# Performance work log

Hardware: AMD Instinct MI355X
Metric: run time of the kernel (lower is better)

## Reference

```python
import jax, jax.numpy as jnp
import numpy as np

B, N, D = 64, 4096, 256


def setup_inputs() -> dict:
    key = jax.random.key(0)
    k1, k2, k3 = jax.random.split(key, 3)
    x = jax.random.normal(k1, (B, D), dtype=jnp.float32)
    z = jax.random.normal(k2, (B, D), dtype=jnp.float32)
    means = jax.random.normal(k3, (B, N, D), dtype=jnp.float32)
    precision = jnp.eye(D, dtype=jnp.float32)  # matches torch init: nn.Parameter(torch.eye(mem_dim))
    return {"x": x, "z": z, "means": means, "precision": precision, "iterations": 10}


def reference(x, z, means, precision, iterations):
    # EM-like iterative soft-assignment: Mahalanobis distances -> softmax weights -> weighted mean.
    def step(z, _):
        diff = means - z[:, None, :]                                  # [B, N, D]
        quad = jnp.einsum('bnd,de,bne->bn', diff, precision, diff)    # [B, N] quadratic forms
        w = jax.nn.softmax(-0.5 * quad, axis=1)                       # [B, N]
        z_new = jnp.einsum('bn,bnd->bd', w, means)                    # [B, D]
        return z_new, None

    z_final, _ = jax.lax.scan(step, z, None, length=iterations)
    return z_final
```

## Files before the change

kernel.cpp:

```cpp
#include <hip/hip_runtime.h>
#include <hip/hip_fp16.h>
#include <hip/hip_cooperative_groups.h>
#include <math.h>

namespace cg = cooperative_groups;

constexpr int B_ = 64;
constexpr int N_ = 4096;
constexpr int D_ = 256;
constexpr int NCH = 64;
constexpr int NPB = N_ / NCH;
constexpr int NPW = NPB / 4;
constexpr int NSTEP = NPW / 4;

typedef float f4v __attribute__((ext_vector_type(4)));
__device__ __forceinline__ float4 nt_load4(const float4* p) {
    f4v v = __builtin_nontemporal_load((const f4v*)p);
    return make_float4(v.x, v.y, v.z, v.w);
}

__global__ __launch_bounds__(256) void flag_kernel(const float* __restrict__ P,
                                                   int* __restrict__ flag) {
    __shared__ int sh[256];
    const int tid = threadIdx.x;
    int bad = 0;
    for (int i = tid; i < D_ * D_; i += 256) {
        const int r = i >> 8, c = i & 255;
        const float expect = (r == c) ? 1.0f : 0.0f;
        bad |= (P[i] != expect) ? 1 : 0;
    }
    sh[tid] = bad;
    __syncthreads();
    for (int s = 128; s > 0; s >>= 1) {
        if (tid < s) sh[tid] |= sh[tid + s];
        __syncthreads();
    }
    if (tid == 0) *flag = sh[0];
}

#define SCORE_AND_UPDATE()                                                     \
    {                                                                          \
        float p_ = 0.f;                                                        \
        _Pragma("unroll")                                                      \
        for (int j = 0; j < 4; j++) {                                          \
            p_ += m[j].x * (vr[j].x - m[j].x);                                 \
            p_ += m[j].y * (vr[j].y - m[j].y);                                 \
            p_ += m[j].z * (vr[j].z - m[j].z);                                 \
            p_ += m[j].w * (vr[j].w - m[j].w);                                 \
        }                                                                      \
        p_ += __shfl_xor(p_, 1, 64);                                           \
        p_ += __shfl_xor(p_, 2, 64);                                           \
        p_ += __shfl_xor(p_, 4, 64);                                           \
        p_ += __shfl_xor(p_, 8, 64);                                           \
        float s_ = 0.5f * p_;                                                  \
        if (flg) {                \
            __syncthreads();                                                   \
            _Pragma("unroll")                                                  \
            for (int jj = 0; jj < 2; jj++)                                     \
                _Pragma("unroll")                                              \
                for (int h = 0; h < 2; h++)                                    \
                    ((float4*)&srows[wave][g][0])[q * 2 + 32 * jj + h] =       \
                        m[jj * 2 + h];                                         \
            __syncthreads();                                                   \
            float dl = 0.f;                                                    \
            for (int k = 0; k < 16; k++) {                                     \
                const int d_ = q * 16 + k;                                     \
                const float md = srows[wave][g][d_];                           \
                float pm = 0.f;                                                \
                for (int e = 0; e < D_; e++)                                   \
                    pm += P[d_ * D_ + e] * srows[wave][g][e];                  \
                dl += md * (md - pm);                                          \
            }                                                                  \
            dl += __shfl_xor(dl, 1, 64);                                       \
            dl += __shfl_xor(dl, 2, 64);                                       \
            dl += __shfl_xor(dl, 4, 64);                                       \
            dl += __shfl_xor(dl, 8, 64);                                       \
            s_ += 0.5f * dl;                                                   \
        }                                                                      \
        const float newM_ = fmaxf(runM, s_);                                   \
        const float sc_ = __expf(runM - newM_);                                \
        const float e_  = __expf(s_ - newM_);                                  \
        runS = fmaf(runS, sc_, e_);                                            \
        _Pragma("unroll")                                                      \
        for (int j = 0; j < 4; j++) {                                          \
            tacc[j].x = fmaf(tacc[j].x, sc_, e_ * m[j].x);                     \
            tacc[j].y = fmaf(tacc[j].y, sc_, e_ * m[j].y);                     \
            tacc[j].z = fmaf(tacc[j].z, sc_, e_ * m[j].z);                     \
            tacc[j].w = fmaf(tacc[j].w, sc_, e_ * m[j].w);                     \
        }                                                                      \
        runM = newM_;                                                          \
    }

#define FAST_SCORE_UPDATE()                                                    \
    {                                                                          \
        float p_ = 0.f;                                                        \
        _Pragma("unroll")                                                      \
        for (int j = 0; j < 4; j++) {                                          \
            p_ += m[j].x * (vr[j].x - m[j].x);                                 \
            p_ += m[j].y * (vr[j].y - m[j].y);                                 \
            p_ += m[j].z * (vr[j].z - m[j].z);                                 \
            p_ += m[j].w * (vr[j].w - m[j].w);                                 \
        }                                                                      \
        p_ += __shfl_xor(p_, 1, 64);                                           \
        p_ += __shfl_xor(p_, 2, 64);                                           \
        p_ += __shfl_xor(p_, 4, 64);                                           \
        p_ += __shfl_xor(p_, 8, 64);                                           \
        const float s_ = 0.5f * p_;                                            \
        const float newM_ = fmaxf(runM, s_);                                   \
        const float sc_ = __expf(runM - newM_);                                \
        const float e_  = __expf(s_ - newM_);                                  \
        runS = fmaf(runS, sc_, e_);                                            \
        _Pragma("unroll")                                                      \
        for (int j = 0; j < 4; j++) {                                          \
            tacc[j].x = fmaf(tacc[j].x, sc_, e_ * m[j].x);                     \
            tacc[j].y = fmaf(tacc[j].y, sc_, e_ * m[j].y);                     \
            tacc[j].z = fmaf(tacc[j].z, sc_, e_ * m[j].z);                     \
            tacc[j].w = fmaf(tacc[j].w, sc_, e_ * m[j].w);                     \
        }                                                                      \
        runM = newM_;                                                          \
    }

template <bool USE_H, int PARTS_>
__global__ __launch_bounds__(256) void persistent_kernel(
        const float* __restrict__ means, const float* __restrict__ z0,
        const float* __restrict__ P, const int* __restrict__ flag,
        __half* __restrict__ mh, float* __restrict__ pT,
        float2* __restrict__ pS, float* __restrict__ out) {
    constexpr int GRID = 64 * PARTS_;
    constexpr int RPB = N_ / PARTS_;
    constexpr int RPW = RPB / 4;
    constexpr int NSTEPS = RPW / 4;
    cg::grid_group grid = cg::this_grid();

    const int gid = blockIdx.x, bb = gid / PARTS_, part = gid % PARTS_;
    const int tid = threadIdx.x, wave = tid >> 6, lane = tid & 63;
    const int q = lane & 15, g = lane >> 4;

    __shared__ __align__(16) float vsh[D_];
    __shared__ __align__(16) float shbuf[4][D_];
    __shared__ __align__(16) float srows[4][4][D_];
    __shared__ __align__(16) float zsh[D_];
    __shared__ float wM[4], wS[4];

    const int flg = *flag;

    {
        const float zd = z0[bb * D_ + tid];
        if (!flg) {
            vsh[tid] = 2.f * zd;
        } else {
            zsh[tid] = zd;
            __syncthreads();
            float vv = 0.f;
            for (int e = 0; e < D_; e++)
                vv += (P[tid * D_ + e] + P[e * D_ + tid]) * zsh[e];
            vsh[tid] = vv;
        }
        __syncthreads();
    }

    const size_t wrowbase = (size_t)bb * N_ + (size_t)part * RPB + (size_t)wave * RPW;

    for (int t = 0; t < 10; t++) {
        float4 vr[4];
        #pragma unroll
        for (int jj = 0; jj < 2; jj++)
            #pragma unroll
            for (int h = 0; h < 2; h++)
                vr[jj * 2 + h] = ((const float4*)vsh)[q * 2 + 32 * jj + h];

        float runM = -INFINITY, runS = 0.f;
        float4 tacc[4];
        #pragma unroll
        for (int j = 0; j < 4; j++) tacc[j] = make_float4(0.f, 0.f, 0.f, 0.f);

        if (!flg) {
            if (USE_H && t > 0) {
                const __half* wb = mh + wrowbase * D_;
                float4 r0 = ((const float4*)(wb + (size_t)g * D_))[q];
                float4 r1 = ((const float4*)(wb + (size_t)g * D_))[q + 16];
                #pragma unroll 2
                for (int step = 0; step < NSTEPS; step++) {
                    const int pr = ((step + 1 < NSTEPS) ? step + 1 : step) * 4 + g;
                    const __half* rpn = wb + (size_t)pr * D_;
                    const float4 n0 = ((const float4*)rpn)[q];
                    const float4 n1 = ((const float4*)rpn)[q + 16];
                    float4 m[4];
                    {
                        const __half2* h0 = (const __half2*)&r0;
                        const float2 f0 = __half22float2(h0[0]);
                        const float2 f1 = __half22float2(h0[1]);
                        const float2 f2 = __half22float2(h0[2]);
                        const float2 f3 = __half22float2(h0[3]);
                        m[0] = make_float4(f0.x, f0.y, f1.x, f1.y);
                        m[1] = make_float4(f2.x, f2.y, f3.x, f3.y);
                        const __half2* h1 = (const __half2*)&r1;
                        const float2 g0 = __half22float2(h1[0]);
                        const float2 g1 = __half22float2(h1[1]);
                        const float2 g2 = __half22float2(h1[2]);
                        const float2 g3 = __half22float2(h1[3]);
                        m[2] = make_float4(g0.x, g0.y, g1.x, g1.y);
                        m[3] = make_float4(g2.x, g2.y, g3.x, g3.y);
                    }
                    FAST_SCORE_UPDATE()
                    r0 = n0; r1 = n1;
                }
            } else {
                const float* wb = means + wrowbase * D_;
                float4 m[4];
                {
                    const float4* rp = (const float4*)(wb + (size_t)g * D_);
                    m[0] = nt_load4(rp + q * 2);
                    m[1] = nt_load4(rp + q * 2 + 1);
                    m[2] = nt_load4(rp + q * 2 + 32);
                    m[3] = nt_load4(rp + q * 2 + 33);
                }
                #pragma unroll 2
                for (int step = 0; step < NSTEPS; step++) {
                    const int pr = ((step + 1 < NSTEPS) ? step + 1 : step) * 4 + g;
                    const float4* rpn = (const float4*)(wb + (size_t)pr * D_);
                    const float4 n0 = nt_load4(rpn + q * 2);
                    const float4 n1 = nt_load4(rpn + q * 2 + 1);
                    const float4 n2 = nt_load4(rpn + q * 2 + 32);
                    const float4 n3 = nt_load4(rpn + q * 2 + 33);
                    if (USE_H && t == 0) {
                        const int r = step * 4 + g;
                        __half* hp = mh + (wrowbase + r) * D_;
                        #pragma unroll
                        for (int jj = 0; jj < 2; jj++) {
                            union { uint4 u4; __half2 h2[4]; } pk;
                            pk.h2[0] = __floats2half2_rn(m[jj*2].x,   m[jj*2].y);
                            pk.h2[1] = __floats2half2_rn(m[jj*2].z,   m[jj*2].w);
                            pk.h2[2] = __floats2half2_rn(m[jj*2+1].x, m[jj*2+1].y);
                            pk.h2[3] = __floats2half2_rn(m[jj*2+1].z, m[jj*2+1].w);
                            *(uint4*)(hp + q * 8 + 128 * jj) = pk.u4;
                        }
                    }
                    FAST_SCORE_UPDATE()
                    m[0] = n0; m[1] = n1; m[2] = n2; m[3] = n3;
                }
            }
        } else {
            if (USE_H && t > 0) {
                for (int step = 0; step < NSTEPS; step++) {
                    const int r = step * 4 + g;
                    const __half* rp = mh + (wrowbase + r) * D_;
                    float4 m[4];
                    #pragma unroll
                    for (int jj = 0; jj < 2; jj++) {
                        float4 raw = ((const float4*)rp)[q + 16 * jj];
                        const __half2* hp2 = (const __half2*)&raw;
                        const float2 f0 = __half22float2(hp2[0]);
                        const float2 f1 = __half22float2(hp2[1]);
                        const float2 f2 = __half22float2(hp2[2]);
                        const float2 f3 = __half22float2(hp2[3]);
                        m[jj * 2 + 0] = make_float4(f0.x, f0.y, f1.x, f1.y);
                        m[jj * 2 + 1] = make_float4(f2.x, f2.y, f3.x, f3.y);
                    }
                    SCORE_AND_UPDATE()
                }
            } else {
                for (int step = 0; step < NSTEPS; step++) {
                    const int r = step * 4 + g;
                    const float* rp = means + (wrowbase + r) * D_;
                    float4 m[4];
                    #pragma unroll
                    for (int jj = 0; jj < 2; jj++)
                        #pragma unroll
                        for (int h = 0; h < 2; h++)
                            m[jj * 2 + h] = ((const float4*)rp)[q * 2 + 32 * jj + h];
                    if (USE_H && t == 0) {
                        __half* hp = mh + (wrowbase + r) * D_;
                        #pragma unroll
                        for (int jj = 0; jj < 2; jj++) {
                            union { uint4 u4; __half2 h2[4]; } pk;
                            pk.h2[0] = __floats2half2_rn(m[jj*2].x,   m[jj*2].y);
                            pk.h2[1] = __floats2half2_rn(m[jj*2].z,   m[jj*2].w);
                            pk.h2[2] = __floats2half2_rn(m[jj*2+1].x, m[jj*2+1].y);
                            pk.h2[3] = __floats2half2_rn(m[jj*2+1].z, m[jj*2+1].w);
                            *(uint4*)(hp + q * 8 + 128 * jj) = pk.u4;
                        }
                    }
                    SCORE_AND_UPDATE()
                }
            }
        }

        float Mw = runM;
        Mw = fmaxf(Mw, __shfl_xor(Mw, 16, 64));
        Mw = fmaxf(Mw, __shfl_xor(Mw, 32, 64));
        const float aw = __expf(runM - Mw);
        float Sa = runS * aw;
        Sa += __shfl_xor(Sa, 16, 64);
        Sa += __shfl_xor(Sa, 32, 64);
        #pragma unroll
        for (int j = 0; j < 4; j++) {
            tacc[j].x *= aw; tacc[j].y *= aw; tacc[j].z *= aw; tacc[j].w *= aw;
            tacc[j].x += __shfl_xor(tacc[j].x, 16, 64);
            tacc[j].y += __shfl_xor(tacc[j].y, 16, 64);
            tacc[j].z += __shfl_xor(tacc[j].z, 16, 64);
            tacc[j].w += __shfl_xor(tacc[j].w, 16, 64);
            tacc[j].x += __shfl_xor(tacc[j].x, 32, 64);
            tacc[j].y += __shfl_xor(tacc[j].y, 32, 64);
            tacc[j].z += __shfl_xor(tacc[j].z, 32, 64);
            tacc[j].w += __shfl_xor(tacc[j].w, 32, 64);
        }
        if (lane < 16) {
            #pragma unroll
            for (int j = 0; j < 4; j++)
                ((float4*)shbuf[wave])[q * 2 + 32 * (j >> 1) + (j & 1)] = tacc[j];
        }
        if (lane == 0) { wM[wave] = Mw; wS[wave] = Sa; }
        __syncthreads();
        const float Mb = fmaxf(fmaxf(wM[0], wM[1]), fmaxf(wM[2], wM[3]));
        const float a0 = __expf(wM[0] - Mb), a1 = __expf(wM[1] - Mb),
                    a2 = __expf(wM[2] - Mb), a3 = __expf(wM[3] - Mb);
        const float Tc = a0 * shbuf[0][tid] + a1 * shbuf[1][tid] +
                         a2 * shbuf[2][tid] + a3 * shbuf[3][tid];
        const int buf = t & 1;
        pT[((size_t)buf * GRID + gid) * D_ + tid] = Tc;
        if (tid == 0)
            pS[buf * GRID + gid] = make_float2(
                Mb, a0 * wS[0] + a1 * wS[1] + a2 * wS[2] + a3 * wS[3]);

        grid.sync();

        float Mg = -INFINITY;
        float2 stl[PARTS_];
        #pragma unroll
        for (int pI = 0; pI < PARTS_; pI++) {
            stl[pI] = pS[buf * GRID + bb * PARTS_ + pI];
            Mg = fmaxf(Mg, stl[pI].x);
        }
        float Sg = 0.f, accg = 0.f;
        #pragma unroll
        for (int pI = 0; pI < PARTS_; pI++) {
            const float a = __expf(stl[pI].x - Mg);
            Sg += a * stl[pI].y;
            accg += a * pT[((size_t)buf * GRID + bb * PARTS_ + pI) * D_ + tid];
        }
        const float zv = accg / Sg;
        if (t == 9) {
            if (part == 0) out[bb * D_ + tid] = zv;
        } else {
            if (!flg) {
                vsh[tid] = 2.f * zv;
            } else {
                zsh[tid] = zv;
                __syncthreads();
                float vv = 0.f;
                for (int e = 0; e < D_; e++)
                    vv += (P[tid * D_ + e] + P[e * D_ + tid]) * zsh[e];
                vsh[tid] = vv;
            }
            __syncthreads();
        }
    }
}

__global__ __launch_bounds__(256) void vcalc_kernel(const float* __restrict__ P,
                                                    const float* __restrict__ z,
                                                    const int* __restrict__ flag,
                                                    float* __restrict__ v) {
    __shared__ float zsh[D_];
    const int b = blockIdx.x, d = threadIdx.x;
    const float zd = z[b * D_ + d];
    if (*flag == 0) {
        v[b * D_ + d] = 2.0f * zd;
        return;
    }
    zsh[d] = zd;
    __syncthreads();
    float acc = 0.f;
    for (int e = 0; e < D_; e++)
        acc += (P[d * D_ + e] + P[e * D_ + d]) * zsh[e];
    v[b * D_ + d] = acc;
}

template <bool WRITE_H>
__global__ __launch_bounds__(256) void fused_f32_kernel(const float* __restrict__ means,
                                                        const float* __restrict__ v,
                                                        const float* __restrict__ P,
                                                        const int* __restrict__ flag,
                                                        __half* __restrict__ mh,
                                                        float* __restrict__ Tbuf,
                                                        float2* __restrict__ stats) {
    const int b = blockIdx.y, chunk = blockIdx.x;
    const int tid = threadIdx.x, wave = tid >> 6, lane = tid & 63;
    const int q = lane & 15, g = lane >> 4;
    __shared__ __align__(16) float vsh[D_];
    __shared__ __align__(16) float shbuf[4][D_];
    __shared__ __align__(16) float srows[4][4][D_];
    __shared__ float wM[4], wS[4];
    vsh[tid] = v[b * D_ + tid];
    __syncthreads();
    float4 vr[4];
    #pragma unroll
    for (int jj = 0; jj < 2; jj++)
        #pragma unroll
        for (int h = 0; h < 2; h++)
            vr[jj * 2 + h] = ((const float4*)vsh)[q * 2 + 32 * jj + h];
    const int flg = *flag;

    float runM = -INFINITY, runS = 0.f;
    float4 tacc[4];
    #pragma unroll
    for (int j = 0; j < 4; j++) tacc[j] = make_float4(0.f, 0.f, 0.f, 0.f);

    const size_t rowbase = (size_t)b * N_ + (size_t)chunk * NPB + (size_t)wave * NPW;

    for (int step = 0; step < NSTEP; step++) {
        const int r = step * 4 + g;
        const float* rp = means + (rowbase + r) * D_;
        float4 m[4];
        #pragma unroll
        for (int jj = 0; jj < 2; jj++)
            #pragma unroll
            for (int h = 0; h < 2; h++)
                m[jj * 2 + h] = ((const float4*)rp)[q * 2 + 32 * jj + h];
        if (WRITE_H) {
            __half* hp = mh + (rowbase + r) * D_;
            #pragma unroll
            for (int jj = 0; jj < 2; jj++) {
                union { uint4 u4; __half2 h2[4]; } pk;
                pk.h2[0] = __floats2half2_rn(m[jj*2].x,   m[jj*2].y);
                pk.h2[1] = __floats2half2_rn(m[jj*2].z,   m[jj*2].w);
                pk.h2[2] = __floats2half2_rn(m[jj*2+1].x, m[jj*2+1].y);
                pk.h2[3] = __floats2half2_rn(m[jj*2+1].z, m[jj*2+1].w);
                *(uint4*)(hp + q * 8 + 128 * jj) = pk.u4;
            }
        }
        SCORE_AND_UPDATE()
    }

    float Mw = runM;
    Mw = fmaxf(Mw, __shfl_xor(Mw, 16, 64));
    Mw = fmaxf(Mw, __shfl_xor(Mw, 32, 64));
    const float aw = __expf(runM - Mw);
    float Sa = runS * aw;
    Sa += __shfl_xor(Sa, 16, 64);
    Sa += __shfl_xor(Sa, 32, 64);
    #pragma unroll
    for (int j = 0; j < 4; j++) {
        tacc[j].x *= aw; tacc[j].y *= aw; tacc[j].z *= aw; tacc[j].w *= aw;
        tacc[j].x += __shfl_xor(tacc[j].x, 16, 64);
        tacc[j].y += __shfl_xor(tacc[j].y, 16, 64);
        tacc[j].z += __shfl_xor(tacc[j].z, 16, 64);
        tacc[j].w += __shfl_xor(tacc[j].w, 16, 64);
        tacc[j].x += __shfl_xor(tacc[j].x, 32, 64);
        tacc[j].y += __shfl_xor(tacc[j].y, 32, 64);
        tacc[j].z += __shfl_xor(tacc[j].z, 32, 64);
        tacc[j].w += __shfl_xor(tacc[j].w, 32, 64);
    }
    if (lane < 16) {
        #pragma unroll
        for (int j = 0; j < 4; j++)
            ((float4*)shbuf[wave])[q * 2 + 32 * (j >> 1) + (j & 1)] = tacc[j];
    }
    if (lane == 0) { wM[wave] = Mw; wS[wave] = Sa; }
    __syncthreads();
    const float Mb = fmaxf(fmaxf(wM[0], wM[1]), fmaxf(wM[2], wM[3]));
    const float a0 = __expf(wM[0] - Mb), a1 = __expf(wM[1] - Mb),
                a2 = __expf(wM[2] - Mb), a3 = __expf(wM[3] - Mb);
    const float Tc = a0 * shbuf[0][tid] + a1 * shbuf[1][tid] +
                     a2 * shbuf[2][tid] + a3 * shbuf[3][tid];
    Tbuf[((size_t)(b * NCH + chunk)) * D_ + tid] = Tc;
    if (tid == 0)
        stats[b * NCH + chunk] = make_float2(
            Mb, a0 * wS[0] + a1 * wS[1] + a2 * wS[2] + a3 * wS[3]);
}

__global__ __launch_bounds__(256) void fused_f16_kernel(const __half* __restrict__ mh,
                                                        const float* __restrict__ v,
                                                        const float* __restrict__ P,
                                                        const int* __restrict__ flag,
                                                        float* __restrict__ Tbuf,
                                                        float2* __restrict__ stats) {
    const int b = blockIdx.y, chunk = blockIdx.x;
    const int tid = threadIdx.x, wave = tid >> 6, lane = tid & 63;
    const int q = lane & 15, g = lane >> 4;
    __shared__ __align__(16) float vsh[D_];
    __shared__ __align__(16) float shbuf[4][D_];
    __shared__ __align__(16) float srows[4][4][D_];
    __shared__ float wM[4], wS[4];
    vsh[tid] = v[b * D_ + tid];
    __syncthreads();
    float4 vr[4];
    #pragma unroll
    for (int jj = 0; jj < 2; jj++)
        #pragma unroll
        for (int h = 0; h < 2; h++)
            vr[jj * 2 + h] = ((const float4*)vsh)[q * 2 + 32 * jj + h];
    const int flg = *flag;

    float runM = -INFINITY, runS = 0.f;
    float4 tacc[4];
    #pragma unroll
    for (int j = 0; j < 4; j++) tacc[j] = make_float4(0.f, 0.f, 0.f, 0.f);

    const size_t rowbase = (size_t)b * N_ + (size_t)chunk * NPB + (size_t)wave * NPW;

    for (int step = 0; step < NSTEP; step++) {
        const int r = step * 4 + g;
        const __half* rp = mh + (rowbase + r) * D_;
        float4 m[4];
        #pragma unroll
        for (int jj = 0; jj < 2; jj++) {
            float4 raw = ((const float4*)rp)[q + 16 * jj];
            const __half2* hp2 = (const __half2*)&raw;
            const float2 f0 = __half22float2(hp2[0]);
            const float2 f1 = __half22float2(hp2[1]);
            const float2 f2 = __half22float2(hp2[2]);
            const float2 f3 = __half22float2(hp2[3]);
            m[jj * 2 + 0] = make_float4(f0.x, f0.y, f1.x, f1.y);
            m[jj * 2 + 1] = make_float4(f2.x, f2.y, f3.x, f3.y);
        }
        SCORE_AND_UPDATE()
    }

    float Mw = runM;
    Mw = fmaxf(Mw, __shfl_xor(Mw, 16, 64));
    Mw = fmaxf(Mw, __shfl_xor(Mw, 32, 64));
    const float aw = __expf(runM - Mw);
    float Sa = runS * aw;
    Sa += __shfl_xor(Sa, 16, 64);
    Sa += __shfl_xor(Sa, 32, 64);
    #pragma unroll
    for (int j = 0; j < 4; j++) {
        tacc[j].x *= aw; tacc[j].y *= aw; tacc[j].z *= aw; tacc[j].w *= aw;
        tacc[j].x += __shfl_xor(tacc[j].x, 16, 64);
        tacc[j].y += __shfl_xor(tacc[j].y, 16, 64);
        tacc[j].z += __shfl_xor(tacc[j].z, 16, 64);
        tacc[j].w += __shfl_xor(tacc[j].w, 16, 64);
        tacc[j].x += __shfl_xor(tacc[j].x, 32, 64);
        tacc[j].y += __shfl_xor(tacc[j].y, 32, 64);
        tacc[j].z += __shfl_xor(tacc[j].z, 32, 64);
        tacc[j].w += __shfl_xor(tacc[j].w, 32, 64);
    }
    if (lane < 16) {
        #pragma unroll
        for (int j = 0; j < 4; j++)
            ((float4*)shbuf[wave])[q * 2 + 32 * (j >> 1) + (j & 1)] = tacc[j];
    }
    if (lane == 0) { wM[wave] = Mw; wS[wave] = Sa; }
    __syncthreads();
    const float Mb = fmaxf(fmaxf(wM[0], wM[1]), fmaxf(wM[2], wM[3]));
    const float a0 = __expf(wM[0] - Mb), a1 = __expf(wM[1] - Mb),
                a2 = __expf(wM[2] - Mb), a3 = __expf(wM[3] - Mb);
    const float Tc = a0 * shbuf[0][tid] + a1 * shbuf[1][tid] +
                     a2 * shbuf[2][tid] + a3 * shbuf[3][tid];
    Tbuf[((size_t)(b * NCH + chunk)) * D_ + tid] = Tc;
    if (tid == 0)
        stats[b * NCH + chunk] = make_float2(
            Mb, a0 * wS[0] + a1 * wS[1] + a2 * wS[2] + a3 * wS[3]);
}

__global__ __launch_bounds__(256) void combine_kernel(const float* __restrict__ Tbuf,
                                                      const float2* __restrict__ stats,
                                                      const float* __restrict__ P,
                                                      const int* __restrict__ flag,
                                                      float* __restrict__ v,
                                                      float* __restrict__ out) {
    const int b = blockIdx.x, d = threadIdx.x;
    __shared__ float Msh[NCH], Ssh[NCH];
    __shared__ float zsh[D_];
    if (d < NCH) {
        const float2 st = stats[b * NCH + d];
        Msh[d] = st.x; Ssh[d] = st.y;
    }
    __syncthreads();
    float M = -INFINITY;
    for (int c = 0; c < NCH; c++) M = fmaxf(M, Msh[c]);
    float S = 0.f, acc = 0.f;
    for (int c = 0; c < NCH; c++) {
        const float a = __expf(Msh[c] - M);
        S += a * Ssh[c];
        acc += a * Tbuf[((size_t)(b * NCH + c)) * D_ + d];
    }
    const float z = acc / S;
    if (out) out[b * D_ + d] = z;
    if (*flag == 0) {
        v[b * D_ + d] = 2.0f * z;
        return;
    }
    zsh[d] = z;
    __syncthreads();
    float vv = 0.f;
    for (int e = 0; e < D_; e++)
        vv += (P[d * D_ + e] + P[e * D_ + d]) * zsh[e];
    v[b * D_ + d] = vv;
}

extern "C" void kernel_launch(void* const* d_in, const int* in_sizes, int n_in,
                              void* d_out, int out_size, void* d_ws, size_t ws_size,
                              hipStream_t stream) {
    const float* z0    = (const float*)d_in[1];
    const float* means = (const float*)d_in[2];
    const float* P     = (const float*)d_in[3];
    float* out = (float*)d_out;

    char* ws = (char*)d_ws;
    size_t off = 0;
    int*    flag  = (int*)ws;                     off = 256;
    float*  v     = (float*)(ws + off);           off += (size_t)B_ * D_ * 4;
    float*  Tbuf  = (float*)(ws + off);           off += (size_t)B_ * NCH * D_ * 4;
    float2* stats = (float2*)(ws + off);          off += (size_t)B_ * NCH * 8;
    off = (off + 255) & ~(size_t)255;
    float*  pT    = (float*)(ws + off);           off += 2ull * 1024 * D_ * 4;
    float2* pS    = (float2*)(ws + off);          off += 2ull * 1024 * 8;
    off = (off + 255) & ~(size_t)255;
    __half* mh    = (__half*)(ws + off);
    const size_t coop_need  = off;
    const size_t full_need  = off + (size_t)B_ * N_ * D_ * 2;
    const bool use_h = (ws_size >= full_need);
    const bool ws_ok = (ws_size >= coop_need);

    flag_kernel<<<dim3(1), dim3(256), 0, stream>>>(P, flag);

    if (ws_ok) {
        void* args[] = {(void*)&means, (void*)&z0, (void*)&P, (void*)&flag,
                        (void*)&mh, (void*)&pT, (void*)&pS, (void*)&out};
        int nb = 0;
        if (use_h) {
            if (hipOccupancyMaxActiveBlocksPerMultiprocessor(
                    &nb, persistent_kernel<true, 16>, 256, 0) == hipSuccess && nb >= 4) {
                if (hipLaunchCooperativeKernel(persistent_kernel<true, 16>,
                        dim3(1024), dim3(256), args, 0, stream) == hipSuccess)
                    return;
            }
            nb = 0;
            if (hipOccupancyMaxActiveBlocksPerMultiprocessor(
                    &nb, persistent_kernel<true, 8>, 256, 0) == hipSuccess && nb >= 2) {
                if (hipLaunchCooperativeKernel(persistent_kernel<true, 8>,
                        dim3(512), dim3(256), args, 0, stream) == hipSuccess)
                    return;
            }
        } else {
            if (hipOccupancyMaxActiveBlocksPerMultiprocessor(
                    &nb, persistent_kernel<false, 16>, 256, 0) == hipSuccess && nb >= 4) {
                if (hipLaunchCooperativeKernel(persistent_kernel<false, 16>,
                        dim3(1024), dim3(256), args, 0, stream) == hipSuccess)
                    return;
            }
            nb = 0;
            if (hipOccupancyMaxActiveBlocksPerMultiprocessor(
                    &nb, persistent_kernel<false, 8>, 256, 0) == hipSuccess && nb >= 2) {
                if (hipLaunchCooperativeKernel(persistent_kernel<false, 8>,
                        dim3(512), dim3(256), args, 0, stream) == hipSuccess)
                    return;
            }
        }
    }

    vcalc_kernel<<<dim3(B_), dim3(256), 0, stream>>>(P, z0, flag, v);
    if (use_h) {
        fused_f32_kernel<true><<<dim3(NCH, B_), dim3(256), 0, stream>>>(
            means, v, P, flag, mh, Tbuf, stats);
        combine_kernel<<<dim3(B_), dim3(256), 0, stream>>>(Tbuf, stats, P, flag, v, nullptr);
        for (int t = 1; t < 10; t++) {
            fused_f16_kernel<<<dim3(NCH, B_), dim3(256), 0, stream>>>(
                mh, v, P, flag, Tbuf, stats);
            combine_kernel<<<dim3(B_), dim3(256), 0, stream>>>(Tbuf, stats, P, flag, v,
                                                               (t == 9) ? out : nullptr);
        }
    } else {
        for (int t = 0; t < 10; t++) {
            fused_f32_kernel<false><<<dim3(NCH, B_), dim3(256), 0, stream>>>(
                means, v, P, flag, nullptr, Tbuf, stats);
            combine_kernel<<<dim3(B_), dim3(256), 0, stream>>>(Tbuf, stats, P, flag, v,
                                                               (t == 9) ? out : nullptr);
        }
    }
}
```

Baseline: 731.6 us.

## Precompute mᵀPm per row, deepen fp16 prefetch, split FMA chains

Adds a separate kernel that precomputes 0.5·mᵀPm for every mean row when the precision matrix is not the identity. The slow path then needs only a dot product minus that constant, replacing its per-step O(D²) shared-memory matvec and barriers. The identity fast path gets a 4-deep register prefetch of fp16 rows and four independent FMA accumulators to shorten dependency chains. It also sets launch_bounds min-blocks to 4 and removes the srows shared buffer. Since the test uses an identity P, cn_kernel exits early and only the prefetch, FMA and occupancy changes affect timing, at the cost of one extra launch and more register pressure.

After: 1.460 ms. 99.6% more time.

```diff
diff --git a/kernel.cpp b/kernel.cpp
--- a/kernel.cpp
+++ b/kernel.cpp
@@ -12,11 +12,29 @@
 constexpr int NPB = N_ / NCH;
 constexpr int NPW = NPB / 4;
 constexpr int NSTEP = NPW / 4;
+constexpr int CNR = 16;
 
 typedef float f4v __attribute__((ext_vector_type(4)));
 __device__ __forceinline__ float4 nt_load4(const float4* p) {
     f4v v = __builtin_nontemporal_load((const f4v*)p);
     return make_float4(v.x, v.y, v.z, v.w);
+}
+
+__device__ __forceinline__ void cvt_h8(const float4 r0, const float4 r1, float4 m[4]) {
+    const __half2* h0 = (const __half2*)&r0;
+    const float2 f0 = __half22float2(h0[0]);
+    const float2 f1 = __half22float2(h0[1]);
+    const float2 f2 = __half22float2(h0[2]);
+    const float2 f3 = __half22float2(h0[3]);
+    m[0] = make_float4(f0.x, f0.y, f1.x, f1.y);
+    m[1] = make_float4(f2.x, f2.y, f3.x, f3.y);
+    const __half2* h1 = (const __half2*)&r1;
+    const float2 g0 = __half22float2(h1[0]);
+    const float2 g1 = __half22float2(h1[1]);
+    const float2 g2 = __half22float2(h1[2]);
+    const float2 g3 = __half22float2(h1[3]);
+    m[2] = make_float4(g0.x, g0.y, g1.x, g1.y);
+    m[3] = make_float4(g2.x, g2.y, g3.x, g3.y);
 }
 
 __global__ __launch_bounds__(256) void flag_kernel(const float* __restrict__ P,
@@ -37,6 +55,92 @@
     }
     if (tid == 0) *flag = sh[0];
 }
+
+__global__ __launch_bounds__(256) void cn_kernel(const float* __restrict__ means,
+                                                 const float* __restrict__ P,
+                                                 const int* __restrict__ flag,
+                                                 float* __restrict__ Cn) {
+    if (*flag == 0) return;
+    const int row0 = blockIdx.x * CNR;
+    const int d = threadIdx.x;
+    __shared__ __align__(16) float msh[CNR][D_];
+    __shared__ float red[CNR][4];
+    #pragma unroll
+    for (int i = 0; i < CNR; i++)
+        msh[i][d] = means[(size_t)(row0 + i) * D_ + d];
+    __syncthreads();
+    float acc[CNR];
+    #pragma unroll
+    for (int r = 0; r < CNR; r++) acc[r] = 0.f;
+    for (int e = 0; e < D_; e++) {
+        const float pde = P[d * D_ + e];
+        #pragma unroll
+        for (int r = 0; r < CNR; r++) acc[r] = fmaf(pde, msh[r][e], acc[r]);
+    }
+    const int lane = d & 63, wv = d >> 6;
+    #pragma unroll
+    for (int r = 0; r < CNR; r++) {
+        float pv = msh[r][d] * acc[r];
+        for (int s = 1; s < 64; s <<= 1) pv += __shfl_xor(pv, s, 64);
+        if (lane == 0) red[r][wv] = pv;
+    }
+    __syncthreads();
+    if (d < CNR)
+        Cn[row0 + d] = 0.5f * (red[d][0] + red[d][1] + red[d][2] + red[d][3]);
+}
+
+#define REDUCE16(P)                                                            \
+    P += __shfl_xor(P, 1, 64);                                                 \
+    P += __shfl_xor(P, 2, 64);                                                 \
+    P += __shfl_xor(P, 4, 64);                                                 \
+    P += __shfl_xor(P, 8, 64);
+
+#define ONLINE_UPDATE(SEXPR)                                                   \
+    {                                                                          \
+        const float s_ = (SEXPR);                                              \
+        const float newM_ = fmaxf(runM, s_);                                   \
+        const float sc_ = __expf(runM - newM_);                                \
+        const float e_  = __expf(s_ - newM_);                                  \
+        runS = fmaf(runS, sc_, e_);                                            \
+        _Pragma("unroll")                                                      \
+        for (int j = 0; j < 4; j++) {                                          \
+            tacc[j].x = fmaf(tacc[j].x, sc_, e_ * m[j].x);                     \
+            tacc[j].y = fmaf(tacc[j].y, sc_, e_ * m[j].y);                     \
+            tacc[j].z = fmaf(tacc[j].z, sc_, e_ * m[j].z);                     \
+            tacc[j].w = fmaf(tacc[j].w, sc_, e_ * m[j].w);                     \
+        }                                                                      \
+        runM = newM_;                                                          \
+    }
+
+#define FAST_SCORE_UPDATE()                                                    \
+    {                                                                          \
+        float pa = 0.f, pb = 0.f, pc2 = 0.f, pd = 0.f;                         \
+        _Pragma("unroll")                                                      \
+        for (int j = 0; j < 4; j++) {                                          \
+            pa  = fmaf(m[j].x, vr[j].x - m[j].x, pa);                          \
+            pb  = fmaf(m[j].y, vr[j].y - m[j].y, pb);                          \
+            pc2 = fmaf(m[j].z, vr[j].z - m[j].z, pc2);                         \
+            pd  = fmaf(m[j].w, vr[j].w - m[j].w, pd);                          \
+        }                                                                      \
+        float p_ = (pa + pb) + (pc2 + pd);                                     \
+        REDUCE16(p_)                                                           \
+        ONLINE_UPDATE(0.5f * p_)                                               \
+    }
+
+#define SLOW_SCORE_UPDATE(CV)                                                  \
+    {                                                                          \
+        float pa = 0.f, pb = 0.f, pc2 = 0.f, pd = 0.f;                         \
+        _Pragma("unroll")                                                      \
+        for (int j = 0; j < 4; j++) {                                          \
+            pa  = fmaf(m[j].x, vr[j].x, pa);                                   \
+            pb  = fmaf(m[j].y, vr[j].y, pb);                                   \
+            pc2 = fmaf(m[j].z, vr[j].z, pc2);                                  \
+            pd  = fmaf(m[j].w, vr[j].w, pd);                                   \
+        }                                                                      \
+        float p_ = (pa + pb) + (pc2 + pd);                                     \
+        REDUCE16(p_)                                                           \
+        ONLINE_UPDATE(0.5f * p_ - (CV))                                        \
+    }
 
 #define SCORE_AND_UPDATE()                                                     \
     {                                                                          \
@@ -53,7 +157,7 @@
         p_ += __shfl_xor(p_, 4, 64);                                           \
         p_ += __shfl_xor(p_, 8, 64);                                           \
         float s_ = 0.5f * p_;                                                  \
-        if (flg) {                \
+        if (flg) {                                                             \
             __syncthreads();                                                   \
             _Pragma("unroll")                                                  \
             for (int jj = 0; jj < 2; jj++)                                     \
@@ -91,41 +195,13 @@
         runM = newM_;                                                          \
     }
 
-#define FAST_SCORE_UPDATE()                                                    \
-    {                                                                          \
-        float p_ = 0.f;                                                        \
-        _Pragma("unroll")                                                      \
-        for (int j = 0; j < 4; j++) {                                          \
-            p_ += m[j].x * (vr[j].x - m[j].x);                                 \
-            p_ += m[j].y * (vr[j].y - m[j].y);                                 \
-            p_ += m[j].z * (vr[j].z - m[j].z);                                 \
-            p_ += m[j].w * (vr[j].w - m[j].w);                                 \
-        }                                                                      \
-        p_ += __shfl_xor(p_, 1, 64);                                           \
-        p_ += __shfl_xor(p_, 2, 64);                                           \
-        p_ += __shfl_xor(p_, 4, 64);                                           \
-        p_ += __shfl_xor(p_, 8, 64);                                           \
-        const float s_ = 0.5f * p_;                                            \
-        const float newM_ = fmaxf(runM, s_);                                   \
-        const float sc_ = __expf(runM - newM_);                                \
-        const float e_  = __expf(s_ - newM_);                                  \
-        runS = fmaf(runS, sc_, e_);                                            \
-        _Pragma("unroll")                                                      \
-        for (int j = 0; j < 4; j++) {                                          \
-            tacc[j].x = fmaf(tacc[j].x, sc_, e_ * m[j].x);                     \
-            tacc[j].y = fmaf(tacc[j].y, sc_, e_ * m[j].y);                     \
-            tacc[j].z = fmaf(tacc[j].z, sc_, e_ * m[j].z);                     \
-            tacc[j].w = fmaf(tacc[j].w, sc_, e_ * m[j].w);                     \
-        }                                                                      \
-        runM = newM_;                                                          \
-    }
-
 template <bool USE_H, int PARTS_>
-__global__ __launch_bounds__(256) void persistent_kernel(
+__global__ __launch_bounds__(256, 4) void persistent_kernel(
         const float* __restrict__ means, const float* __restrict__ z0,
         const float* __restrict__ P, const int* __restrict__ flag,
-        __half* __restrict__ mh, float* __restrict__ pT,
-        float2* __restrict__ pS, float* __restrict__ out) {
+        const float* __restrict__ Cn, __half* __restrict__ mh,
+        float* __restrict__ pT, float2* __restrict__ pS,
+        float* __restrict__ out) {
     constexpr int GRID = 64 * PARTS_;
     constexpr int RPB = N_ / PARTS_;
     constexpr int RPW = RPB / 4;
@@ -138,7 +214,6 @@
 
     __shared__ __align__(16) float vsh[D_];
     __shared__ __align__(16) float shbuf[4][D_];
-    __shared__ __align__(16) float srows[4][4][D_];
     __shared__ __align__(16) float zsh[D_];
     __shared__ float wM[4], wS[4];
 
@@ -177,52 +252,59 @@
         if (!flg) {
             if (USE_H && t > 0) {
                 const __half* wb = mh + wrowbase * D_;
-                float4 r0 = ((const float4*)(wb + (size_t)g * D_))[q];
-                float4 r1 = ((const float4*)(wb + (size_t)g * D_))[q + 16];
-                #pragma unroll 2
-                for (int step = 0; step < NSTEPS; step++) {
-                    const int pr = ((step + 1 < NSTEPS) ? step + 1 : step) * 4 + g;
-                    const __half* rpn = wb + (size_t)pr * D_;
-                    const float4 n0 = ((const float4*)rpn)[q];
-                    const float4 n1 = ((const float4*)rpn)[q + 16];
-                    float4 m[4];
-                    {
-                        const __half2* h0 = (const __half2*)&r0;
-                        const float2 f0 = __half22float2(h0[0]);
-                        const float2 f1 = __half22float2(h0[1]);
-                        const float2 f2 = __half22float2(h0[2]);
-                        const float2 f3 = __half22float2(h0[3]);
-                        m[0] = make_float4(f0.x, f0.y, f1.x, f1.y);
-                        m[1] = make_float4(f2.x, f2.y, f3.x, f3.y);
-                        const __half2* h1 = (const __half2*)&r1;
-                        const float2 g0 = __half22float2(h1[0]);
-                        const float2 g1 = __half22float2(h1[1]);
-                        const float2 g2 = __half22float2(h1[2]);
-                        const float2 g3 = __half22float2(h1[3]);
-                        m[2] = make_float4(g0.x, g0.y, g1.x, g1.y);
-                        m[3] = make_float4(g2.x, g2.y, g3.x, g3.y);
+                constexpr int PF = 4;
+                float4 pf0[PF], pf1[PF];
+                #pragma unroll
+                for (int i = 0; i < PF; i++) {
+                    const int rr = (i < NSTEPS ? i : NSTEPS - 1) * 4 + g;
+                    const __half* rp = wb + (size_t)rr * D_;
+                    pf0[i] = ((const float4*)rp)[q];
+                    pf1[i] = ((const float4*)rp)[q + 16];
+                }
+                for (int base = 0; base < NSTEPS; base += PF) {
+                    #pragma unroll
+                    for (int k = 0; k < PF; k++) {
+                        const int step = base + k;
+                        const float4 r0 = pf0[k], r1 = pf1[k];
+                        const int ps = (step + PF < NSTEPS) ? step + PF
+                                                            : NSTEPS - 1;
+                        const __half* rp = wb + (size_t)(ps * 4 + g) * D_;
+                        pf0[k] = ((const float4*)rp)[q];
+                        pf1[k] = ((const float4*)rp)[q + 16];
+                        float4 m[4];
+                        cvt_h8(r0, r1, m);
+                        FAST_SCORE_UPDATE()
                     }
-                    FAST_SCORE_UPDATE()
-                    r0 = n0; r1 = n1;
                 }
             } else {
                 const float* wb = means + wrowbase * D_;
                 float4 m[4];
                 {
                     const float4* rp = (const float4*)(wb + (size_t)g * D_);
-                    m[0] = nt_load4(rp + q * 2);
-                    m[1] = nt_load4(rp + q * 2 + 1);
-                    m[2] = nt_load4(rp + q * 2 + 32);
-                    m[3] = nt_load4(rp + q * 2 + 33);
+                    if (USE_H) {
+                        m[0] = nt_load4(rp + q * 2);
+                        m[1] = nt_load4(rp + q * 2 + 1);
+                        m[2] = nt_load4(rp + q * 2 + 32);
+                        m[3] = nt_load4(rp + q * 2 + 33);
+                    } else {
+                        m[0] = rp[q * 2];     m[1] = rp[q * 2 + 1];
+                        m[2] = rp[q * 2 + 32]; m[3] = rp[q * 2 + 33];
+                    }
                 }
                 #pragma unroll 2
                 for (int step = 0; step < NSTEPS; step++) {
                     const int pr = ((step + 1 < NSTEPS) ? step + 1 : step) * 4 + g;
                     const float4* rpn = (const float4*)(wb + (size_t)pr * D_);
-                    const float4 n0 = nt_load4(rpn + q * 2);
-                    const float4 n1 = nt_load4(rpn + q * 2 + 1);
-                    const float4 n2 = nt_load4(rpn + q * 2 + 32);
-                    const float4 n3 = nt_load4(rpn + q * 2 + 33);
+                    float4 n0, n1, n2, n3;
+                    if (USE_H) {
+                        n0 = nt_load4(rpn + q * 2);
+                        n1 = nt_load4(rpn + q * 2 + 1);
+                        n2 = nt_load4(rpn + q * 2 + 32);
+                        n3 = nt_load4(rpn + q * 2 + 33);
+                    } else {
+                        n0 = rpn[q * 2];     n1 = rpn[q * 2 + 1];
+                        n2 = rpn[q * 2 + 32]; n3 = rpn[q * 2 + 33];
+                    }
                     if (USE_H && t == 0) {
                         const int r = step * 4 + g;
                         __half* hp = mh + (wrowbase + r) * D_;
@@ -245,19 +327,12 @@
                 for (int step = 0; step < NSTEPS; step++) {
                     const int r = step * 4 + g;
                     const __half* rp = mh + (wrowbase + r) * D_;
+                    const float4 r0 = ((const float4*)rp)[q];
+                    const float4 r1 = ((const float4*)rp)[q + 16];
                     float4 m[4];
-                    #pragma unroll
-                    for (int jj = 0; jj < 2; jj++) {
-                        float4 raw = ((const float4*)rp)[q + 16 * jj];
-                        const __half2* hp2 = (const __half2*)&raw;
-                        const float2 f0 = __half22float2(hp2[0]);
-                        const float2 f1 = __half22float2(hp2[1]);
-                        const float2 f2 = __half22float2(hp2[2]);
-                        const float2 f3 = __half22float2(hp2[3]);
-                        m[jj * 2 + 0] = make_float4(f0.x, f0.y, f1.x, f1.y);
-                        m[jj * 2 + 1] = make_float4(f2.x, f2.y, f3.x, f3.y);
-                    }
-                    SCORE_AND_UPDATE()
+                    cvt_h8(r0, r1, m);
+                    const float cv = Cn[wrowbase + r];
+                    SLOW_SCORE_UPDATE(cv)
                 }
             } else {
                 for (int step = 0; step < NSTEPS; step++) {
@@ -281,7 +356,8 @@
                             *(uint4*)(hp + q * 8 + 128 * jj) = pk.u4;
                         }
                     }
-                    SCORE_AND_UPDATE()
+                    const float cv = Cn[wrowbase + r];
+                    SLOW_SCORE_UPDATE(cv)
                 }
             }
         }
@@ -609,6 +685,8 @@
     float*  pT    = (float*)(ws + off);           off += 2ull * 1024 * D_ * 4;
     float2* pS    = (float2*)(ws + off);          off += 2ull * 1024 * 8;
     off = (off + 255) & ~(size_t)255;
+    float*  Cn    = (float*)(ws + off);           off += (size_t)B_ * N_ * 4;
+    off = (off + 255) & ~(size_t)255;
     __half* mh    = (__half*)(ws + off);
     const size_t coop_need  = off;
     const size_t full_need  = off + (size_t)B_ * N_ * D_ * 2;
@@ -618,8 +696,10 @@
     flag_kernel<<<dim3(1), dim3(256), 0, stream>>>(P, flag);
 
     if (ws_ok) {
+        cn_kernel<<<dim3(B_ * N_ / CNR), dim3(256), 0, stream>>>(means, P, flag, Cn);
+
         void* args[] = {(void*)&means, (void*)&z0, (void*)&P, (void*)&flag,
-                        (void*)&mh, (void*)&pT, (void*)&pS, (void*)&out};
+                        (void*)&Cn, (void*)&mh, (void*)&pT, (void*)&pS, (void*)&out};
         int nb = 0;
         if (use_h) {
             if (hipOccupancyMaxActiveBlocksPerMultiprocessor(
```
